# Optimization experiments

Measured on AMD Instinct MI355X. Metric: run time of the kernel, lower is better.

## Reference

```python
import jax, jax.numpy as jnp
import numpy as np

N_POINTS = 2_000_000
N_VOXELS = 1_500_000
N_SP = 50_000
C = 32
LN_EPS = 1e-5  # torch nn.LayerNorm default


def setup_inputs() -> dict:
    key = jax.random.key(0)
    ks = jax.random.split(key, 8)
    voxel_feats = jax.random.normal(ks[0], (N_VOXELS, C), jnp.float32)
    xyz = jax.random.normal(ks[1], (N_POINTS, 3), jnp.float32)
    p2v_map = jax.random.randint(ks[2], (N_POINTS,), 0, N_VOXELS, dtype=jnp.int32)
    sp_ids = jax.random.randint(ks[3], (N_POINTS,), 0, N_SP, dtype=jnp.int32)
    W1 = jax.random.normal(ks[4], (3, C), jnp.float32) * (1.0 / np.sqrt(3.0))
    b1 = jnp.zeros((C,), jnp.float32)
    gamma = jnp.ones((C,), jnp.float32)
    beta = jnp.zeros((C,), jnp.float32)
    W2 = jax.random.normal(ks[5], (C, C), jnp.float32) * (1.0 / np.sqrt(C))
    b2 = jnp.zeros((C,), jnp.float32)
    return {
        'voxel_feats': voxel_feats, 'xyz': xyz,
        'W1': W1, 'b1': b1, 'gamma': gamma, 'beta': beta, 'W2': W2, 'b2': b2,
        'p2v_map': p2v_map, 'sp_ids': sp_ids, 'num_superpoints': N_SP,
    }


def reference(voxel_feats, xyz, W1, b1, gamma, beta, W2, b2, p2v_map, sp_ids, num_superpoints):
    # gather voxel features to points: x = voxel_feats[p2v_map]  [N_pts, C]
    x = voxel_feats[p2v_map]

    # pos_encode MLP: Linear(3,32) -> LayerNorm(32) -> ReLU -> Linear(32,32)
    h = xyz @ W1 + b1
    mu = jnp.mean(h, axis=-1, keepdims=True)
    var = jnp.mean(jnp.square(h - mu), axis=-1, keepdims=True)
    h = (h - mu) * jax.lax.rsqrt(var + LN_EPS) * gamma + beta
    x_pos = jax.nn.relu(h) @ W2 + b2

    # scatter(reduce='mean') into superpoints; compute counts once
    counts = jax.ops.segment_sum(jnp.ones((xyz.shape[0],), x.dtype), sp_ids,
                                 num_segments=num_superpoints)
    denom = jnp.maximum(counts, 1.0)[:, None]

    def smean(v):
        return jax.ops.segment_sum(v, sp_ids, num_segments=num_superpoints) / denom

    x_sp = smean(x) + smean(x_pos)          # [S, C]
    sp_xyz = smean(xyz)                      # [S, 3]
    return (x_sp, sp_xyz)
```

## Files before the change

kernel.cpp:

```cpp
#include <hip/hip_runtime.h>
#include <hip/hip_bf16.h>

#define C 32
#define LN_EPS 1e-5f
#define P 8
#define SCAN_BLK 1024

__device__ __forceinline__ unsigned pack_bf16x2(float a, float b) {
    __hip_bfloat162 bb = __float22bfloat162_rn(make_float2(a, b));
    return *reinterpret_cast<unsigned*>(&bb);
}

__global__ __launch_bounds__(256) void kA1_rank_mlp(
    const float* __restrict__ voxel_feats,
    const float* __restrict__ xyz,
    const float* __restrict__ W1, const float* __restrict__ b1,
    const float* __restrict__ gamma, const float* __restrict__ beta,
    const float* __restrict__ W2, const float* __restrict__ b2,
    const int* __restrict__ p2v, const int* __restrict__ sp_ids,
    int* __restrict__ count, int* __restrict__ rank,
    uint4* __restrict__ y_s,
    int n)
{
    int p = blockIdx.x * 256 + threadIdx.x;
    if (p >= n) return;

    int sp = sp_ids[p];
    rank[p] = atomicAdd(&count[sp], 1);

    int v = p2v[p];
    const float4* vrow = (const float4*)(voxel_feats + (size_t)v * C);
    float4 g0 = vrow[0], g1 = vrow[1], g2 = vrow[2], g3 = vrow[3];
    float4 g4 = vrow[4], g5 = vrow[5], g6 = vrow[6], g7 = vrow[7];

    float x0 = xyz[3 * p + 0];
    float x1 = xyz[3 * p + 1];
    float x2 = xyz[3 * p + 2];

    float h[C];
    #pragma unroll
    for (int c = 0; c < C; ++c)
        h[c] = fmaf(x0, W1[c], fmaf(x1, W1[C + c], fmaf(x2, W1[2 * C + c], b1[c])));

    float s = 0.f, s2 = 0.f;
    #pragma unroll
    for (int c = 0; c < C; ++c) { s += h[c]; s2 += h[c] * h[c]; }
    float mu   = s * (1.0f / C);
    float var  = fmaf(-mu, mu, s2 * (1.0f / C));
    float rstd = rsqrtf(var + LN_EPS);
    #pragma unroll
    for (int c = 0; c < C; ++c)
        h[c] = fmaxf(fmaf((h[c] - mu) * rstd, gamma[c], beta[c]), 0.0f);

    float acc[C];
    #pragma unroll
    for (int c = 0; c < C; ++c) acc[c] = b2[c];
    #pragma unroll
    for (int k = 0; k < C; ++k) {
        float rk = h[k];
        #pragma unroll
        for (int c = 0; c < C; ++c)
            acc[c] = fmaf(rk, W2[k * C + c], acc[c]);
    }

    float gf[C] = { g0.x,g0.y,g0.z,g0.w, g1.x,g1.y,g1.z,g1.w,
                    g2.x,g2.y,g2.z,g2.w, g3.x,g3.y,g3.z,g3.w,
                    g4.x,g4.y,g4.z,g4.w, g5.x,g5.y,g5.z,g5.w,
                    g6.x,g6.y,g6.z,g6.w, g7.x,g7.y,g7.z,g7.w };
    #pragma unroll
    for (int c = 0; c < C; ++c) acc[c] += gf[c];

    uint4 y0, y1, y2, y3;
    y0.x = pack_bf16x2(acc[0],  acc[1]);  y0.y = pack_bf16x2(acc[2],  acc[3]);
    y0.z = pack_bf16x2(acc[4],  acc[5]);  y0.w = pack_bf16x2(acc[6],  acc[7]);
    y1.x = pack_bf16x2(acc[8],  acc[9]);  y1.y = pack_bf16x2(acc[10], acc[11]);
    y1.z = pack_bf16x2(acc[12], acc[13]); y1.w = pack_bf16x2(acc[14], acc[15]);
    y2.x = pack_bf16x2(acc[16], acc[17]); y2.y = pack_bf16x2(acc[18], acc[19]);
    y2.z = pack_bf16x2(acc[20], acc[21]); y2.w = pack_bf16x2(acc[22], acc[23]);
    y3.x = pack_bf16x2(acc[24], acc[25]); y3.y = pack_bf16x2(acc[26], acc[27]);
    y3.z = pack_bf16x2(acc[28], acc[29]); y3.w = pack_bf16x2(acc[30], acc[31]);
    uint4* dst = y_s + (size_t)p * 4;
    dst[0] = y0; dst[1] = y1; dst[2] = y2; dst[3] = y3;
}

__global__ __launch_bounds__(SCAN_BLK) void k2a_scan_block(
    const int* __restrict__ count, int* __restrict__ off,
    int* __restrict__ bsum, int S)
{
    __shared__ int lds[SCAN_BLK];
    int t = threadIdx.x;
    int i = blockIdx.x * SCAN_BLK + t;
    int v = (i < S) ? count[i] : 0;
    lds[t] = v;
    __syncthreads();
    for (int d = 1; d < SCAN_BLK; d <<= 1) {
        int add = (t >= d) ? lds[t - d] : 0;
        __syncthreads();
        lds[t] += add;
        __syncthreads();
    }
    int incl = lds[t];
    if (i < S) off[i] = incl - v;
    if (t == SCAN_BLK - 1) bsum[blockIdx.x] = incl;
}

__global__ __launch_bounds__(64) void k2b_scan_bsums(int* __restrict__ bsum, int nb)
{
    int lane = threadIdx.x;
    int v = (lane < nb) ? bsum[lane] : 0;
    int own = v;
    for (int d = 1; d < 64; d <<= 1) {
        int u = __shfl_up(v, d, 64);
        if (lane >= d) v += u;
    }
    if (lane < nb) bsum[lane] = v - own;
}

__global__ __launch_bounds__(256) void k2c_add_prefix(
    int* __restrict__ off, const int* __restrict__ bsum, int S)
{
    int i = blockIdx.x * 256 + threadIdx.x;
    if (i >= S) return;
    off[i] += bsum[i / SCAN_BLK];
}

__global__ __launch_bounds__(256) void k3x_scatter16(
    const int* __restrict__ sp_ids, const int* __restrict__ rank,
    const int* __restrict__ off, const float* __restrict__ xyz,
    uint4* __restrict__ xyzp, int n)
{
    int p = blockIdx.x * 256 + threadIdx.x;
    if (p >= n) return;
    int sp = sp_ids[p];
    int j  = off[sp] + rank[p];
    xyzp[j] = make_uint4(__float_as_uint(xyz[3 * p + 0]),
                         __float_as_uint(xyz[3 * p + 1]),
                         __float_as_uint(xyz[3 * p + 2]),
                         (unsigned)p);
}

__global__ __launch_bounds__(256) void kB2_reduce(
    const uint4* __restrict__ y_s,
    const uint4* __restrict__ xyzp,
    const int* __restrict__ off, const int* __restrict__ count,
    float* __restrict__ out_x, float* __restrict__ out_xyz, int S)
{
    int gt  = blockIdx.x * 256 + threadIdx.x;
    int sp  = gt >> 3;
    int sub = gt & 7;
    if (sp >= S) return;

    int n    = count[sp];
    int base = off[sp];

    float acc[C];
    #pragma unroll
    for (int c = 0; c < C; ++c) acc[c] = 0.f;
    float ax = 0.f, ay = 0.f, az = 0.f;

    int i = sub;
    for (; i + P < n; i += 2 * P) {
        uint4 r0 = xyzp[base + i];
        uint4 r1 = xyzp[base + i + P];
        const uint4* q0 = y_s + (size_t)r0.w * 4;
        const uint4* q1 = y_s + (size_t)r1.w * 4;
        uint4 a0 = q0[0], b0 = q0[1], c0 = q0[2], d0 = q0[3];
        uint4 a1 = q1[0], b1_ = q1[1], c1 = q1[2], d1 = q1[3];
        ax += __uint_as_float(r0.x) + __uint_as_float(r1.x);
        ay += __uint_as_float(r0.y) + __uint_as_float(r1.y);
        az += __uint_as_float(r0.z) + __uint_as_float(r1.z);
        unsigned w0[16] = { a0.x,a0.y,a0.z,a0.w, b0.x,b0.y,b0.z,b0.w,
                            c0.x,c0.y,c0.z,c0.w, d0.x,d0.y,d0.z,d0.w };
        unsigned w1[16] = { a1.x,a1.y,a1.z,a1.w, b1_.x,b1_.y,b1_.z,b1_.w,
                            c1.x,c1.y,c1.z,c1.w, d1.x,d1.y,d1.z,d1.w };
        #pragma unroll
        for (int q = 0; q < 16; ++q) {
            acc[2 * q + 0] += __uint_as_float(w0[q] << 16) + __uint_as_float(w1[q] << 16);
            acc[2 * q + 1] += __uint_as_float(w0[q] & 0xFFFF0000u) + __uint_as_float(w1[q] & 0xFFFF0000u);
        }
    }
    if (i < n) {
        uint4 r0 = xyzp[base + i];
        const uint4* q0 = y_s + (size_t)r0.w * 4;
        uint4 a0 = q0[0], b0 = q0[1], c0 = q0[2], d0 = q0[3];
        ax += __uint_as_float(r0.x);
        ay += __uint_as_float(r0.y);
        az += __uint_as_float(r0.z);
        unsigned w0[16] = { a0.x,a0.y,a0.z,a0.w, b0.x,b0.y,b0.z,b0.w,
                            c0.x,c0.y,c0.z,c0.w, d0.x,d0.y,d0.z,d0.w };
        #pragma unroll
        for (int q = 0; q < 16; ++q) {
            acc[2 * q + 0] += __uint_as_float(w0[q] << 16);
            acc[2 * q + 1] += __uint_as_float(w0[q] & 0xFFFF0000u);
        }
    }

    #pragma unroll
    for (int c = 0; c < C; ++c) {
        acc[c] += __shfl_xor(acc[c], 1);
        acc[c] += __shfl_xor(acc[c], 2);
        acc[c] += __shfl_xor(acc[c], 4);
    }
    ax += __shfl_xor(ax, 1); ax += __shfl_xor(ax, 2); ax += __shfl_xor(ax, 4);
    ay += __shfl_xor(ay, 1); ay += __shfl_xor(ay, 2); ay += __shfl_xor(ay, 4);
    az += __shfl_xor(az, 1); az += __shfl_xor(az, 2); az += __shfl_xor(az, 4);

    if (sub == 0) {
        float inv = 1.0f / fmaxf((float)n, 1.0f);
        float4* o4 = (float4*)(out_x + (size_t)sp * C);
        #pragma unroll
        for (int q = 0; q < 8; ++q) {
            float4 f;
            f.x = acc[4 * q + 0] * inv;
            f.y = acc[4 * q + 1] * inv;
            f.z = acc[4 * q + 2] * inv;
            f.w = acc[4 * q + 3] * inv;
            o4[q] = f;
        }
        out_xyz[3 * sp + 0] = ax * inv;
        out_xyz[3 * sp + 1] = ay * inv;
        out_xyz[3 * sp + 2] = az * inv;
    }
}

__global__ __launch_bounds__(256) void k3_reorder(
    const int* __restrict__ sp_ids, const int* __restrict__ rank,
    const int* __restrict__ off, int* __restrict__ order, int n)
{
    int p = blockIdx.x * 256 + threadIdx.x;
    if (p >= n) return;
    order[off[sp_ids[p]] + rank[p]] = p;
}

__global__ __launch_bounds__(256) void kB_gather_reduce(
    const uint4* __restrict__ y_s, const float* __restrict__ xyz,
    const int* __restrict__ order,
    const int* __restrict__ off, const int* __restrict__ count,
    float* __restrict__ out_x, float* __restrict__ out_xyz, int S)
{
    int gt = blockIdx.x * 256 + threadIdx.x;
    int sp = gt >> 3, sub = gt & 7;
    if (sp >= S) return;
    int n = count[sp], base = off[sp];
    float acc[C];
    #pragma unroll
    for (int c = 0; c < C; ++c) acc[c] = 0.f;
    float ax = 0.f, ay = 0.f, az = 0.f;
    for (int i = sub; i < n; i += P) {
        int o = order[base + i];
        const uint4* r = y_s + (size_t)o * 4;
        uint4 a = r[0], b = r[1], c4 = r[2], d = r[3];
        const float* xp = xyz + 3 * (size_t)o;
        ax += xp[0]; ay += xp[1]; az += xp[2];
        unsigned w[16] = { a.x,a.y,a.z,a.w, b.x,b.y,b.z,b.w,
                           c4.x,c4.y,c4.z,c4.w, d.x,d.y,d.z,d.w };
        #pragma unroll
        for (int q = 0; q < 16; ++q) {
            acc[2 * q + 0] += __uint_as_float(w[q] << 16);
            acc[2 * q + 1] += __uint_as_float(w[q] & 0xFFFF0000u);
        }
    }
    #pragma unroll
    for (int c = 0; c < C; ++c) {
        acc[c] += __shfl_xor(acc[c], 1);
        acc[c] += __shfl_xor(acc[c], 2);
        acc[c] += __shfl_xor(acc[c], 4);
    }
    ax += __shfl_xor(ax, 1); ax += __shfl_xor(ax, 2); ax += __shfl_xor(ax, 4);
    ay += __shfl_xor(ay, 1); ay += __shfl_xor(ay, 2); ay += __shfl_xor(ay, 4);
    az += __shfl_xor(az, 1); az += __shfl_xor(az, 2); az += __shfl_xor(az, 4);
    if (sub == 0) {
        float inv = 1.0f / fmaxf((float)n, 1.0f);
        float4* o4 = (float4*)(out_x + (size_t)sp * C);
        #pragma unroll
        for (int q = 0; q < 8; ++q) {
            float4 f;
            f.x = acc[4 * q + 0] * inv; f.y = acc[4 * q + 1] * inv;
            f.z = acc[4 * q + 2] * inv; f.w = acc[4 * q + 3] * inv;
            o4[q] = f;
        }
        out_xyz[3 * sp + 0] = ax * inv;
        out_xyz[3 * sp + 1] = ay * inv;
        out_xyz[3 * sp + 2] = az * inv;
    }
}

extern "C" void kernel_launch(void* const* d_in, const int* in_sizes, int n_in,
                              void* d_out, int out_size, void* d_ws, size_t ws_size,
                              hipStream_t stream)
{
    const float* voxel_feats = (const float*)d_in[0];
    const float* xyz         = (const float*)d_in[1];
    const float* W1          = (const float*)d_in[2];
    const float* b1          = (const float*)d_in[3];
    const float* gamma       = (const float*)d_in[4];
    const float* beta        = (const float*)d_in[5];
    const float* W2          = (const float*)d_in[6];
    const float* b2          = (const float*)d_in[7];
    const int*   p2v         = (const int*)d_in[8];
    const int*   sp_ids      = (const int*)d_in[9];

    const int n_pts = in_sizes[8];
    const int S     = out_size / 35;

    float* out_x   = (float*)d_out;
    float* out_xyz = out_x + (size_t)S * C;

    int* count = (int*)d_ws;
    int* off   = count + S;
    int* bsum  = off + S;
    int* rank  = bsum + 64;

    size_t head_b = ((size_t)2 * S + 64 + (size_t)n_pts) * sizeof(int);
    head_b = (head_b + 255) & ~(size_t)255;
    size_t xyzp_b = (size_t)n_pts * 16;
    size_t y_b    = (size_t)n_pts * 64;

    int blk = 256;
    int gpts = (n_pts + blk - 1) / blk;
    int nb = (S + SCAN_BLK - 1) / SCAN_BLK;
    int n_thr = S * P;

    hipMemsetAsync(count, 0, (size_t)S * sizeof(int), stream);

    if (ws_size >= head_b + xyzp_b + y_b) {
        uint4* xyzp = (uint4*)((char*)d_ws + head_b);
        uint4* y_s  = (uint4*)((char*)d_ws + head_b + xyzp_b);

        kA1_rank_mlp<<<gpts, blk, 0, stream>>>(
            voxel_feats, xyz, W1, b1, gamma, beta, W2, b2,
            p2v, sp_ids, count, rank, y_s, n_pts);
        k2a_scan_block<<<nb, SCAN_BLK, 0, stream>>>(count, off, bsum, S);
        k2b_scan_bsums<<<1, 64, 0, stream>>>(bsum, nb);
        k2c_add_prefix<<<(S + blk - 1) / blk, blk, 0, stream>>>(off, bsum, S);
        k3x_scatter16<<<gpts, blk, 0, stream>>>(sp_ids, rank, off, xyz, xyzp, n_pts);
        kB2_reduce<<<(n_thr + blk - 1) / blk, blk, 0, stream>>>(
            y_s, xyzp, off, count, out_x, out_xyz, S);
    } else {
        int* order = rank + n_pts;
        size_t head5_b = ((size_t)2 * S + 64 + (size_t)2 * n_pts) * sizeof(int);
        head5_b = (head5_b + 255) & ~(size_t)255;
        uint4* y_s = (uint4*)((char*)d_ws + head5_b);

        kA1_rank_mlp<<<gpts, blk, 0, stream>>>(
            voxel_feats, xyz, W1, b1, gamma, beta, W2, b2,
            p2v, sp_ids, count, rank, y_s, n_pts);
        k2a_scan_block<<<nb, SCAN_BLK, 0, stream>>>(count, off, bsum, S);
        k2b_scan_bsums<<<1, 64, 0, stream>>>(bsum, nb);
        k2c_add_prefix<<<(S + blk - 1) / blk, blk, 0, stream>>>(off, bsum, S);
        k3_reorder<<<gpts, blk, 0, stream>>>(sp_ids, rank, off, order, n_pts);
        kB_gather_reduce<<<(n_thr + blk - 1) / blk, blk, 0, stream>>>(
            y_s, xyz, order, off, count, out_x, out_xyz, S);
    }
}
```

Before: 519.1 us.

## Histogram first, then write MLP outputs directly into superpoint-sorted order

Adds a histogram pass over sp_ids and runs the scan before the MLP. The MLP kernel then claims a sorted slot through an atomic cursor and writes its bf16 row and the xyz record straight into segment-contiguous positions. The reduce kernel streams contiguous rows instead of gathering through a permutation index, which removes the separate scatter kernel and the rank array. In exchange it adds an extra pass over sp_ids, and the MLP kernel now makes scattered writes instead of coalesced ones.

```diff
diff --git a/kernel.cpp b/kernel.cpp
--- a/kernel.cpp
+++ b/kernel.cpp
@@ -11,7 +11,220 @@
     return *reinterpret_cast<unsigned*>(&bb);
 }
 
-__global__ __launch_bounds__(256) void kA1_rank_mlp(
+__global__ __launch_bounds__(256) void k0_hist(
+    const int* __restrict__ sp_ids, int* __restrict__ count, int n)
+{
+    int p = blockIdx.x * 256 + threadIdx.x;
+    if (p < n) atomicAdd(&count[sp_ids[p]], 1);
+}
+
+__global__ __launch_bounds__(SCAN_BLK) void k2a_scan_block(
+    const int* __restrict__ count, int* __restrict__ off,
+    int* __restrict__ bsum, int S)
+{
+    __shared__ int lds[SCAN_BLK];
+    int t = threadIdx.x;
+    int i = blockIdx.x * SCAN_BLK + t;
+    int v = (i < S) ? count[i] : 0;
+    lds[t] = v;
+    __syncthreads();
+    for (int d = 1; d < SCAN_BLK; d <<= 1) {
+        int add = (t >= d) ? lds[t - d] : 0;
+        __syncthreads();
+        lds[t] += add;
+        __syncthreads();
+    }
+    int incl = lds[t];
+    if (i < S) off[i] = incl - v;
+    if (t == SCAN_BLK - 1) bsum[blockIdx.x] = incl;
+}
+
+__global__ __launch_bounds__(64) void k2b_scan_bsums(int* __restrict__ bsum, int nb)
+{
+    int lane = threadIdx.x;
+    int v = (lane < nb) ? bsum[lane] : 0;
+    int own = v;
+    for (int d = 1; d < 64; d <<= 1) {
+        int u = __shfl_up(v, d, 64);
+        if (lane >= d) v += u;
+    }
+    if (lane < nb) bsum[lane] = v - own;
+}
+
+__global__ __launch_bounds__(256) void k2c_add_prefix(
+    int* __restrict__ off, const int* __restrict__ bsum,
+    int* __restrict__ cursor, int S)
+{
+    int i = blockIdx.x * 256 + threadIdx.x;
+    if (i >= S) return;
+    int o = off[i] + bsum[i / SCAN_BLK];
+    off[i] = o;
+    if (cursor) cursor[i] = o;
+}
+
+__global__ __launch_bounds__(256) void kA2_mlp_scatter(
+    const float* __restrict__ voxel_feats,
+    const float* __restrict__ xyz,
+    const float* __restrict__ W1, const float* __restrict__ b1,
+    const float* __restrict__ gamma, const float* __restrict__ beta,
+    const float* __restrict__ W2, const float* __restrict__ b2,
+    const int* __restrict__ p2v, const int* __restrict__ sp_ids,
+    int* __restrict__ cursor,
+    uint4* __restrict__ y_s,
+    uint4* __restrict__ xyzp,
+    int n)
+{
+    int p = blockIdx.x * 256 + threadIdx.x;
+    if (p >= n) return;
+
+    int sp = sp_ids[p];
+    int j = atomicAdd(&cursor[sp], 1);
+
+    int v = p2v[p];
+    const float4* vrow = (const float4*)(voxel_feats + (size_t)v * C);
+    float4 g0 = vrow[0], g1 = vrow[1], g2 = vrow[2], g3 = vrow[3];
+    float4 g4 = vrow[4], g5 = vrow[5], g6 = vrow[6], g7 = vrow[7];
+
+    float x0 = xyz[3 * p + 0];
+    float x1 = xyz[3 * p + 1];
+    float x2 = xyz[3 * p + 2];
+
+    float h[C];
+    #pragma unroll
+    for (int c = 0; c < C; ++c)
+        h[c] = fmaf(x0, W1[c], fmaf(x1, W1[C + c], fmaf(x2, W1[2 * C + c], b1[c])));
+
+    float s = 0.f, s2 = 0.f;
+    #pragma unroll
+    for (int c = 0; c < C; ++c) { s += h[c]; s2 += h[c] * h[c]; }
+    float mu   = s * (1.0f / C);
+    float var  = fmaf(-mu, mu, s2 * (1.0f / C));
+    float rstd = rsqrtf(var + LN_EPS);
+    #pragma unroll
+    for (int c = 0; c < C; ++c)
+        h[c] = fmaxf(fmaf((h[c] - mu) * rstd, gamma[c], beta[c]), 0.0f);
+
+    float acc[C];
+    #pragma unroll
+    for (int c = 0; c < C; ++c) acc[c] = b2[c];
+    #pragma unroll
+    for (int k = 0; k < C; ++k) {
+        float rk = h[k];
+        #pragma unroll
+        for (int c = 0; c < C; ++c)
+            acc[c] = fmaf(rk, W2[k * C + c], acc[c]);
+    }
+
+    float gf[C] = { g0.x,g0.y,g0.z,g0.w, g1.x,g1.y,g1.z,g1.w,
+                    g2.x,g2.y,g2.z,g2.w, g3.x,g3.y,g3.z,g3.w,
+                    g4.x,g4.y,g4.z,g4.w, g5.x,g5.y,g5.z,g5.w,
+                    g6.x,g6.y,g6.z,g6.w, g7.x,g7.y,g7.z,g7.w };
+    #pragma unroll
+    for (int c = 0; c < C; ++c) acc[c] += gf[c];
+
+    uint4 y0, y1, y2, y3;
+    y0.x = pack_bf16x2(acc[0],  acc[1]);  y0.y = pack_bf16x2(acc[2],  acc[3]);
+    y0.z = pack_bf16x2(acc[4],  acc[5]);  y0.w = pack_bf16x2(acc[6],  acc[7]);
+    y1.x = pack_bf16x2(acc[8],  acc[9]);  y1.y = pack_bf16x2(acc[10], acc[11]);
+    y1.z = pack_bf16x2(acc[12], acc[13]); y1.w = pack_bf16x2(acc[14], acc[15]);
+    y2.x = pack_bf16x2(acc[16], acc[17]); y2.y = pack_bf16x2(acc[18], acc[19]);
+    y2.z = pack_bf16x2(acc[20], acc[21]); y2.w = pack_bf16x2(acc[22], acc[23]);
+    y3.x = pack_bf16x2(acc[24], acc[25]); y3.y = pack_bf16x2(acc[26], acc[27]);
+    y3.z = pack_bf16x2(acc[28], acc[29]); y3.w = pack_bf16x2(acc[30], acc[31]);
+    uint4* dst = y_s + (size_t)j * 4;
+    dst[0] = y0; dst[1] = y1; dst[2] = y2; dst[3] = y3;
+
+    xyzp[j] = make_uint4(__float_as_uint(x0), __float_as_uint(x1),
+                         __float_as_uint(x2), (unsigned)p);
+}
+
+__global__ __launch_bounds__(256) void kB3_stream_reduce(
+    const uint4* __restrict__ y_s,
+    const uint4* __restrict__ xyzp,
+    const int* __restrict__ off, const int* __restrict__ count,
+    float* __restrict__ out_x, float* __restrict__ out_xyz, int S)
+{
+    int gt  = blockIdx.x * 256 + threadIdx.x;
+    int sp  = gt >> 3;
+    int sub = gt & 7;
+    if (sp >= S) return;
+
+    int n    = count[sp];
+    int base = off[sp];
+
+    float acc[C];
+    #pragma unroll
+    for (int c = 0; c < C; ++c) acc[c] = 0.f;
+    float ax = 0.f, ay = 0.f, az = 0.f;
+
+    int i = sub;
+    for (; i + P < n; i += 2 * P) {
+        int j0 = base + i, j1 = base + i + P;
+        const uint4* q0 = y_s + (size_t)j0 * 4;
+        const uint4* q1 = y_s + (size_t)j1 * 4;
+        uint4 a0 = q0[0], b0 = q0[1], c0 = q0[2], d0 = q0[3];
+        uint4 a1 = q1[0], b1_ = q1[1], c1 = q1[2], d1 = q1[3];
+        uint4 r0 = xyzp[j0];
+        uint4 r1 = xyzp[j1];
+        ax += __uint_as_float(r0.x) + __uint_as_float(r1.x);
+        ay += __uint_as_float(r0.y) + __uint_as_float(r1.y);
+        az += __uint_as_float(r0.z) + __uint_as_float(r1.z);
+        unsigned w0[16] = { a0.x,a0.y,a0.z,a0.w, b0.x,b0.y,b0.z,b0.w,
+                            c0.x,c0.y,c0.z,c0.w, d0.x,d0.y,d0.z,d0.w };
+        unsigned w1[16] = { a1.x,a1.y,a1.z,a1.w, b1_.x,b1_.y,b1_.z,b1_.w,
+                            c1.x,c1.y,c1.z,c1.w, d1.x,d1.y,d1.z,d1.w };
+        #pragma unroll
+        for (int q = 0; q < 16; ++q) {
+            acc[2 * q + 0] += __uint_as_float(w0[q] << 16) + __uint_as_float(w1[q] << 16);
+            acc[2 * q + 1] += __uint_as_float(w0[q] & 0xFFFF0000u) + __uint_as_float(w1[q] & 0xFFFF0000u);
+        }
+    }
+    if (i < n) {
+        int j0 = base + i;
+        const uint4* q0 = y_s + (size_t)j0 * 4;
+        uint4 a0 = q0[0], b0 = q0[1], c0 = q0[2], d0 = q0[3];
+        uint4 r0 = xyzp[j0];
+        ax += __uint_as_float(r0.x);
+        ay += __uint_as_float(r0.y);
+        az += __uint_as_float(r0.z);
+        unsigned w0[16] = { a0.x,a0.y,a0.z,a0.w, b0.x,b0.y,b0.z,b0.w,
+                            c0.x,c0.y,c0.z,c0.w, d0.x,d0.y,d0.z,d0.w };
+        #pragma unroll
+        for (int q = 0; q < 16; ++q) {
+            acc[2 * q + 0] += __uint_as_float(w0[q] << 16);
+            acc[2 * q + 1] += __uint_as_float(w0[q] & 0xFFFF0000u);
+        }
+    }
+
+    #pragma unroll
+    for (int c = 0; c < C; ++c) {
+        acc[c] += __shfl_xor(acc[c], 1);
+        acc[c] += __shfl_xor(acc[c], 2);
+        acc[c] += __shfl_xor(acc[c], 4);
+    }
+    ax += __shfl_xor(ax, 1); ax += __shfl_xor(ax, 2); ax += __shfl_xor(ax, 4);
+    ay += __shfl_xor(ay, 1); ay += __shfl_xor(ay, 2); ay += __shfl_xor(ay, 4);
+    az += __shfl_xor(az, 1); az += __shfl_xor(az, 2); az += __shfl_xor(az, 4);
+
+    if (sub == 0) {
+        float inv = 1.0f / fmaxf((float)n, 1.0f);
+        float4* o4 = (float4*)(out_x + (size_t)sp * C);
+        #pragma unroll
+        for (int q = 0; q < 8; ++q) {
+            float4 f;
+            f.x = acc[4 * q + 0] * inv;
+            f.y = acc[4 * q + 1] * inv;
+            f.z = acc[4 * q + 2] * inv;
+            f.w = acc[4 * q + 3] * inv;
+            o4[q] = f;
+        }
+        out_xyz[3 * sp + 0] = ax * inv;
+        out_xyz[3 * sp + 1] = ay * inv;
+        out_xyz[3 * sp + 2] = az * inv;
+    }
+}
+
+__global__ __launch_bounds__(256) void kA1_rank_mlp_seq(
     const float* __restrict__ voxel_feats,
     const float* __restrict__ xyz,
     const float* __restrict__ W1, const float* __restrict__ b1,
@@ -19,39 +232,30 @@
     const float* __restrict__ W2, const float* __restrict__ b2,
     const int* __restrict__ p2v, const int* __restrict__ sp_ids,
     int* __restrict__ count, int* __restrict__ rank,
-    uint4* __restrict__ y_s,
-    int n)
+    uint4* __restrict__ y_s, int n)
 {
     int p = blockIdx.x * 256 + threadIdx.x;
     if (p >= n) return;
-
     int sp = sp_ids[p];
     rank[p] = atomicAdd(&count[sp], 1);
-
     int v = p2v[p];
     const float4* vrow = (const float4*)(voxel_feats + (size_t)v * C);
     float4 g0 = vrow[0], g1 = vrow[1], g2 = vrow[2], g3 = vrow[3];
     float4 g4 = vrow[4], g5 = vrow[5], g6 = vrow[6], g7 = vrow[7];
-
-    float x0 = xyz[3 * p + 0];
-    float x1 = xyz[3 * p + 1];
-    float x2 = xyz[3 * p + 2];
-
+    float x0 = xyz[3 * p + 0], x1 = xyz[3 * p + 1], x2 = xyz[3 * p + 2];
     float h[C];
     #pragma unroll
     for (int c = 0; c < C; ++c)
         h[c] = fmaf(x0, W1[c], fmaf(x1, W1[C + c], fmaf(x2, W1[2 * C + c], b1[c])));
-
     float s = 0.f, s2 = 0.f;
     #pragma unroll
     for (int c = 0; c < C; ++c) { s += h[c]; s2 += h[c] * h[c]; }
-    float mu   = s * (1.0f / C);
-    float var  = fmaf(-mu, mu, s2 * (1.0f / C));
+    float mu = s * (1.0f / C);
+    float var = fmaf(-mu, mu, s2 * (1.0f / C));
     float rstd = rsqrtf(var + LN_EPS);
     #pragma unroll
     for (int c = 0; c < C; ++c)
         h[c] = fmaxf(fmaf((h[c] - mu) * rstd, gamma[c], beta[c]), 0.0f);
-
     float acc[C];
     #pragma unroll
     for (int c = 0; c < C; ++c) acc[c] = b2[c];
@@ -59,17 +263,14 @@
     for (int k = 0; k < C; ++k) {
         float rk = h[k];
         #pragma unroll
-        for (int c = 0; c < C; ++c)
-            acc[c] = fmaf(rk, W2[k * C + c], acc[c]);
-    }
-
+        for (int c = 0; c < C; ++c) acc[c] = fmaf(rk, W2[k * C + c], acc[c]);
+    }
     float gf[C] = { g0.x,g0.y,g0.z,g0.w, g1.x,g1.y,g1.z,g1.w,
                     g2.x,g2.y,g2.z,g2.w, g3.x,g3.y,g3.z,g3.w,
                     g4.x,g4.y,g4.z,g4.w, g5.x,g5.y,g5.z,g5.w,
                     g6.x,g6.y,g6.z,g6.w, g7.x,g7.y,g7.z,g7.w };
     #pragma unroll
     for (int c = 0; c < C; ++c) acc[c] += gf[c];
-
     uint4 y0, y1, y2, y3;
     y0.x = pack_bf16x2(acc[0],  acc[1]);  y0.y = pack_bf16x2(acc[2],  acc[3]);
     y0.z = pack_bf16x2(acc[4],  acc[5]);  y0.w = pack_bf16x2(acc[6],  acc[7]);
@@ -83,146 +284,6 @@
     dst[0] = y0; dst[1] = y1; dst[2] = y2; dst[3] = y3;
 }
 
-__global__ __launch_bounds__(SCAN_BLK) void k2a_scan_block(
-    const int* __restrict__ count, int* __restrict__ off,
-    int* __restrict__ bsum, int S)
-{
-    __shared__ int lds[SCAN_BLK];
-    int t = threadIdx.x;
-    int i = blockIdx.x * SCAN_BLK + t;
-    int v = (i < S) ? count[i] : 0;
-    lds[t] = v;
-    __syncthreads();
-    for (int d = 1; d < SCAN_BLK; d <<= 1) {
-        int add = (t >= d) ? lds[t - d] : 0;
-        __syncthreads();
-        lds[t] += add;
-        __syncthreads();
-    }
-    int incl = lds[t];
-    if (i < S) off[i] = incl - v;
-    if (t == SCAN_BLK - 1) bsum[blockIdx.x] = incl;
-}
-
-__global__ __launch_bounds__(64) void k2b_scan_bsums(int* __restrict__ bsum, int nb)
-{
-    int lane = threadIdx.x;
-    int v = (lane < nb) ? bsum[lane] : 0;
-    int own = v;
-    for (int d = 1; d < 64; d <<= 1) {
-        int u = __shfl_up(v, d, 64);
-        if (lane >= d) v += u;
-    }
-    if (lane < nb) bsum[lane] = v - own;
-}
-
-__global__ __launch_bounds__(256) void k2c_add_prefix(
-    int* __restrict__ off, const int* __restrict__ bsum, int S)
-{
-    int i = blockIdx.x * 256 + threadIdx.x;
-    if (i >= S) return;
-    off[i] += bsum[i / SCAN_BLK];
-}
-
-__global__ __launch_bounds__(256) void k3x_scatter16(
-    const int* __restrict__ sp_ids, const int* __restrict__ rank,
-    const int* __restrict__ off, const float* __restrict__ xyz,
-    uint4* __restrict__ xyzp, int n)
-{
-    int p = blockIdx.x * 256 + threadIdx.x;
-    if (p >= n) return;
-    int sp = sp_ids[p];
-    int j  = off[sp] + rank[p];
-    xyzp[j] = make_uint4(__float_as_uint(xyz[3 * p + 0]),
-                         __float_as_uint(xyz[3 * p + 1]),
-                         __float_as_uint(xyz[3 * p + 2]),
-                         (unsigned)p);
-}
-
-__global__ __launch_bounds__(256) void kB2_reduce(
-    const uint4* __restrict__ y_s,
-    const uint4* __restrict__ xyzp,
-    const int* __restrict__ off, const int* __restrict__ count,
-    float* __restrict__ out_x, float* __restrict__ out_xyz, int S)
-{
-    int gt  = blockIdx.x * 256 + threadIdx.x;
-    int sp  = gt >> 3;
-    int sub = gt & 7;
-    if (sp >= S) return;
-
-    int n    = count[sp];
-    int base = off[sp];
-
-    float acc[C];
-    #pragma unroll
-    for (int c = 0; c < C; ++c) acc[c] = 0.f;
-    float ax = 0.f, ay = 0.f, az = 0.f;
-
-    int i = sub;
-    for (; i + P < n; i += 2 * P) {
-        uint4 r0 = xyzp[base + i];
-        uint4 r1 = xyzp[base + i + P];
-        const uint4* q0 = y_s + (size_t)r0.w * 4;
-        const uint4* q1 = y_s + (size_t)r1.w * 4;
-        uint4 a0 = q0[0], b0 = q0[1], c0 = q0[2], d0 = q0[3];
-        uint4 a1 = q1[0], b1_ = q1[1], c1 = q1[2], d1 = q1[3];
-        ax += __uint_as_float(r0.x) + __uint_as_float(r1.x);
-        ay += __uint_as_float(r0.y) + __uint_as_float(r1.y);
-        az += __uint_as_float(r0.z) + __uint_as_float(r1.z);
-        unsigned w0[16] = { a0.x,a0.y,a0.z,a0.w, b0.x,b0.y,b0.z,b0.w,
-                            c0.x,c0.y,c0.z,c0.w, d0.x,d0.y,d0.z,d0.w };
-        unsigned w1[16] = { a1.x,a1.y,a1.z,a1.w, b1_.x,b1_.y,b1_.z,b1_.w,
-                            c1.x,c1.y,c1.z,c1.w, d1.x,d1.y,d1.z,d1.w };
-        #pragma unroll
-        for (int q = 0; q < 16; ++q) {
-            acc[2 * q + 0] += __uint_as_float(w0[q] << 16) + __uint_as_float(w1[q] << 16);
-            acc[2 * q + 1] += __uint_as_float(w0[q] & 0xFFFF0000u) + __uint_as_float(w1[q] & 0xFFFF0000u);
-        }
-    }
-    if (i < n) {
-        uint4 r0 = xyzp[base + i];
-        const uint4* q0 = y_s + (size_t)r0.w * 4;
-        uint4 a0 = q0[0], b0 = q0[1], c0 = q0[2], d0 = q0[3];
-        ax += __uint_as_float(r0.x);
-        ay += __uint_as_float(r0.y);
-        az += __uint_as_float(r0.z);
-        unsigned w0[16] = { a0.x,a0.y,a0.z,a0.w, b0.x,b0.y,b0.z,b0.w,
-                            c0.x,c0.y,c0.z,c0.w, d0.x,d0.y,d0.z,d0.w };
-        #pragma unroll
-        for (int q = 0; q < 16; ++q) {
-            acc[2 * q + 0] += __uint_as_float(w0[q] << 16);
-            acc[2 * q + 1] += __uint_as_float(w0[q] & 0xFFFF0000u);
-        }
-    }
-
-    #pragma unroll
-    for (int c = 0; c < C; ++c) {
-        acc[c] += __shfl_xor(acc[c], 1);
-        acc[c] += __shfl_xor(acc[c], 2);
-        acc[c] += __shfl_xor(acc[c], 4);
-    }
-    ax += __shfl_xor(ax, 1); ax += __shfl_xor(ax, 2); ax += __shfl_xor(ax, 4);
-    ay += __shfl_xor(ay, 1); ay += __shfl_xor(ay, 2); ay += __shfl_xor(ay, 4);
-    az += __shfl_xor(az, 1); az += __shfl_xor(az, 2); az += __shfl_xor(az, 4);
-
-    if (sub == 0) {
-        float inv = 1.0f / fmaxf((float)n, 1.0f);
-        float4* o4 = (float4*)(out_x + (size_t)sp * C);
-        #pragma unroll
-        for (int q = 0; q < 8; ++q) {
-            float4 f;
-            f.x = acc[4 * q + 0] * inv;
-            f.y = acc[4 * q + 1] * inv;
-            f.z = acc[4 * q + 2] * inv;
-            f.w = acc[4 * q + 3] * inv;
-            o4[q] = f;
-        }
-        out_xyz[3 * sp + 0] = ax * inv;
-        out_xyz[3 * sp + 1] = ay * inv;
-        out_xyz[3 * sp + 2] = az * inv;
-    }
-}
-
 __global__ __launch_bounds__(256) void k3_reorder(
     const int* __restrict__ sp_ids, const int* __restrict__ rank,
     const int* __restrict__ off, int* __restrict__ order, int n)
@@ -306,48 +367,49 @@
     float* out_x   = (float*)d_out;
     float* out_xyz = out_x + (size_t)S * C;
 
-    int* count = (int*)d_ws;
-    int* off   = count + S;
-    int* bsum  = off + S;
-    int* rank  = bsum + 64;
-
-    size_t head_b = ((size_t)2 * S + 64 + (size_t)n_pts) * sizeof(int);
-    head_b = (head_b + 255) & ~(size_t)255;
-    size_t xyzp_b = (size_t)n_pts * 16;
-    size_t y_b    = (size_t)n_pts * 64;
-
     int blk = 256;
     int gpts = (n_pts + blk - 1) / blk;
     int nb = (S + SCAN_BLK - 1) / SCAN_BLK;
     int n_thr = S * P;
 
+    int* count  = (int*)d_ws;
+    int* off    = count + S;
+    int* bsum   = off + S;
+    int* cursor = bsum + 64;
+
+    size_t head_b = ((size_t)(3 * S) + 64) * sizeof(int);
+    head_b = (head_b + 255) & ~(size_t)255;
+    size_t xyzp_b = (size_t)n_pts * 16;
+    size_t y_b    = (size_t)n_pts * 64;
+
     hipMemsetAsync(count, 0, (size_t)S * sizeof(int), stream);
 
     if (ws_size >= head_b + xyzp_b + y_b) {
         uint4* xyzp = (uint4*)((char*)d_ws + head_b);
         uint4* y_s  = (uint4*)((char*)d_ws + head_b + xyzp_b);
 
-        kA1_rank_mlp<<<gpts, blk, 0, stream>>>(
+        k0_hist<<<gpts, blk, 0, stream>>>(sp_ids, count, n_pts);
+        k2a_scan_block<<<nb, SCAN_BLK, 0, stream>>>(count, off, bsum, S);
+        k2b_scan_bsums<<<1, 64, 0, stream>>>(bsum, nb);
+        k2c_add_prefix<<<(S + blk - 1) / blk, blk, 0, stream>>>(off, bsum, cursor, S);
+        kA2_mlp_scatter<<<gpts, blk, 0, stream>>>(
+            voxel_feats, xyz, W1, b1, gamma, beta, W2, b2,
+            p2v, sp_ids, cursor, y_s, xyzp, n_pts);
+        kB3_stream_reduce<<<(n_thr + blk - 1) / blk, blk, 0, stream>>>(
+            y_s, xyzp, off, count, out_x, out_xyz, S);
+    } else {
+        int* rank  = bsum + 64;
+        int* order = rank + n_pts;
+        size_t head5_b = ((size_t)2 * S + 64 + (size_t)2 * n_pts) * sizeof(int);
+        head5_b = (head5_b + 255) & ~(size_t)255;
+        uint4* y_s = (uint4*)((char*)d_ws + head5_b);
+
+        kA1_rank_mlp_seq<<<gpts, blk, 0, stream>>>(
             voxel_feats, xyz, W1, b1, gamma, beta, W2, b2,
             p2v, sp_ids, count, rank, y_s, n_pts);
         k2a_scan_block<<<nb, SCAN_BLK, 0, stream>>>(count, off, bsum, S);
         k2b_scan_bsums<<<1, 64, 0, stream>>>(bsum, nb);
-        k2c_add_prefix<<<(S + blk - 1) / blk, blk, 0, stream>>>(off, bsum, S);
-        k3x_scatter16<<<gpts, blk, 0, stream>>>(sp_ids, rank, off, xyz, xyzp, n_pts);
-        kB2_reduce<<<(n_thr + blk - 1) / blk, blk, 0, stream>>>(
-            y_s, xyzp, off, count, out_x, out_xyz, S);
-    } else {
-        int* order = rank + n_pts;
-        size_t head5_b = ((size_t)2 * S + 64 + (size_t)2 * n_pts) * sizeof(int);
-        head5_b = (head5_b + 255) & ~(size_t)255;
-        uint4* y_s = (uint4*)((char*)d_ws + head5_b);
-
-        kA1_rank_mlp<<<gpts, blk, 0, stream>>>(
-            voxel_feats, xyz, W1, b1, gamma, beta, W2, b2,
-            p2v, sp_ids, count, rank, y_s, n_pts);
-        k2a_scan_block<<<nb, SCAN_BLK, 0, stream>>>(count, off, bsum, S);
-        k2b_scan_bsums<<<1, 64, 0, stream>>>(bsum, nb);
-        k2c_add_prefix<<<(S + blk - 1) / blk, blk, 0, stream>>>(off, bsum, S);
+        k2c_add_prefix<<<(S + blk - 1) / blk, blk, 0, stream>>>(off, bsum, (int*)nullptr, S);
         k3_reorder<<<gpts, blk, 0, stream>>>(sp_ids, rank, off, order, n_pts);
         kB_gather_reduce<<<(n_thr + blk - 1) / blk, blk, 0, stream>>>(
             y_s, xyz, order, off, count, out_x, out_xyz, S);
```

Result: slower. 613.5 us (+18.2%).

## Fuse pos-MLP and voxel gather into segment reduce, drop bf16 intermediate

Applied to the files above, without the earlier changes.

The MLP and voxel-feature gather move out of a per-point pass that wrote a bf16 per-point buffer and into the per-superpoint reduction kernel. That kernel now reads a packed (xyz, voxel index) record sorted by superpoint and computes the MLP inline. Ranks are now assigned with a cursor atomic in the scatter pass instead of being stored during a histogram pass, so the rank array and the 128MB bf16 buffer are gone. In exchange, the reduction kernel carries heavy per-thread MLP arithmetic with high register pressure, the gather of 128B voxel rows becomes random inside the reduce, and the bf16 rounding of the intermediate is removed.

```diff
diff --git a/kernel.cpp b/kernel.cpp
--- a/kernel.cpp
+++ b/kernel.cpp
@@ -1,86 +1,15 @@
 #include <hip/hip_runtime.h>
-#include <hip/hip_bf16.h>
 
 #define C 32
 #define LN_EPS 1e-5f
 #define P 8
 #define SCAN_BLK 1024
 
-__device__ __forceinline__ unsigned pack_bf16x2(float a, float b) {
-    __hip_bfloat162 bb = __float22bfloat162_rn(make_float2(a, b));
-    return *reinterpret_cast<unsigned*>(&bb);
-}
-
-__global__ __launch_bounds__(256) void kA1_rank_mlp(
-    const float* __restrict__ voxel_feats,
-    const float* __restrict__ xyz,
-    const float* __restrict__ W1, const float* __restrict__ b1,
-    const float* __restrict__ gamma, const float* __restrict__ beta,
-    const float* __restrict__ W2, const float* __restrict__ b2,
-    const int* __restrict__ p2v, const int* __restrict__ sp_ids,
-    int* __restrict__ count, int* __restrict__ rank,
-    uint4* __restrict__ y_s,
-    int n)
+__global__ __launch_bounds__(256) void k0_hist(
+    const int* __restrict__ sp_ids, int* __restrict__ count, int n)
 {
     int p = blockIdx.x * 256 + threadIdx.x;
-    if (p >= n) return;
-
-    int sp = sp_ids[p];
-    rank[p] = atomicAdd(&count[sp], 1);
-
-    int v = p2v[p];
-    const float4* vrow = (const float4*)(voxel_feats + (size_t)v * C);
-    float4 g0 = vrow[0], g1 = vrow[1], g2 = vrow[2], g3 = vrow[3];
-    float4 g4 = vrow[4], g5 = vrow[5], g6 = vrow[6], g7 = vrow[7];
-
-    float x0 = xyz[3 * p + 0];
-    float x1 = xyz[3 * p + 1];
-    float x2 = xyz[3 * p + 2];
-
-    float h[C];
-    #pragma unroll
-    for (int c = 0; c < C; ++c)
-        h[c] = fmaf(x0, W1[c], fmaf(x1, W1[C + c], fmaf(x2, W1[2 * C + c], b1[c])));
-
-    float s = 0.f, s2 = 0.f;
-    #pragma unroll
-    for (int c = 0; c < C; ++c) { s += h[c]; s2 += h[c] * h[c]; }
-    float mu   = s * (1.0f / C);
-    float var  = fmaf(-mu, mu, s2 * (1.0f / C));
-    float rstd = rsqrtf(var + LN_EPS);
-    #pragma unroll
-    for (int c = 0; c < C; ++c)
-        h[c] = fmaxf(fmaf((h[c] - mu) * rstd, gamma[c], beta[c]), 0.0f);
-
-    float acc[C];
-    #pragma unroll
-    for (int c = 0; c < C; ++c) acc[c] = b2[c];
-    #pragma unroll
-    for (int k = 0; k < C; ++k) {
-        float rk = h[k];
-        #pragma unroll
-        for (int c = 0; c < C; ++c)
-            acc[c] = fmaf(rk, W2[k * C + c], acc[c]);
-    }
-
-    float gf[C] = { g0.x,g0.y,g0.z,g0.w, g1.x,g1.y,g1.z,g1.w,
-                    g2.x,g2.y,g2.z,g2.w, g3.x,g3.y,g3.z,g3.w,
-                    g4.x,g4.y,g4.z,g4.w, g5.x,g5.y,g5.z,g5.w,
-                    g6.x,g6.y,g6.z,g6.w, g7.x,g7.y,g7.z,g7.w };
-    #pragma unroll
-    for (int c = 0; c < C; ++c) acc[c] += gf[c];
-
-    uint4 y0, y1, y2, y3;
-    y0.x = pack_bf16x2(acc[0],  acc[1]);  y0.y = pack_bf16x2(acc[2],  acc[3]);
-    y0.z = pack_bf16x2(acc[4],  acc[5]);  y0.w = pack_bf16x2(acc[6],  acc[7]);
-    y1.x = pack_bf16x2(acc[8],  acc[9]);  y1.y = pack_bf16x2(acc[10], acc[11]);
-    y1.z = pack_bf16x2(acc[12], acc[13]); y1.w = pack_bf16x2(acc[14], acc[15]);
-    y2.x = pack_bf16x2(acc[16], acc[17]); y2.y = pack_bf16x2(acc[18], acc[19]);
-    y2.z = pack_bf16x2(acc[20], acc[21]); y2.w = pack_bf16x2(acc[22], acc[23]);
-    y3.x = pack_bf16x2(acc[24], acc[25]); y3.y = pack_bf16x2(acc[26], acc[27]);
-    y3.z = pack_bf16x2(acc[28], acc[29]); y3.w = pack_bf16x2(acc[30], acc[31]);
-    uint4* dst = y_s + (size_t)p * 4;
-    dst[0] = y0; dst[1] = y1; dst[2] = y2; dst[3] = y3;
+    if (p < n) atomicAdd(&count[sp_ids[p]], 1);
 }
 
 __global__ __launch_bounds__(SCAN_BLK) void k2a_scan_block(
@@ -117,31 +46,37 @@
 }
 
 __global__ __launch_bounds__(256) void k2c_add_prefix(
-    int* __restrict__ off, const int* __restrict__ bsum, int S)
+    int* __restrict__ off, const int* __restrict__ bsum,
+    int* __restrict__ cursor, int S)
 {
     int i = blockIdx.x * 256 + threadIdx.x;
     if (i >= S) return;
-    off[i] += bsum[i / SCAN_BLK];
-}
-
-__global__ __launch_bounds__(256) void k3x_scatter16(
-    const int* __restrict__ sp_ids, const int* __restrict__ rank,
-    const int* __restrict__ off, const float* __restrict__ xyz,
-    uint4* __restrict__ xyzp, int n)
+    int o = off[i] + bsum[i / SCAN_BLK];
+    off[i] = o;
+    cursor[i] = o;
+}
+
+__global__ __launch_bounds__(256) void k3v_scatter16(
+    const int* __restrict__ sp_ids, const int* __restrict__ p2v,
+    int* __restrict__ cursor, const float* __restrict__ xyz,
+    uint4* __restrict__ xyzv, int n)
 {
     int p = blockIdx.x * 256 + threadIdx.x;
     if (p >= n) return;
     int sp = sp_ids[p];
-    int j  = off[sp] + rank[p];
-    xyzp[j] = make_uint4(__float_as_uint(xyz[3 * p + 0]),
+    int j  = atomicAdd(&cursor[sp], 1);
+    xyzv[j] = make_uint4(__float_as_uint(xyz[3 * p + 0]),
                          __float_as_uint(xyz[3 * p + 1]),
                          __float_as_uint(xyz[3 * p + 2]),
-                         (unsigned)p);
-}
-
-__global__ __launch_bounds__(256) void kB2_reduce(
-    const uint4* __restrict__ y_s,
-    const uint4* __restrict__ xyzp,
+                         (unsigned)p2v[p]);
+}
+
+__global__ __launch_bounds__(256) void kB4_mlp_reduce(
+    const float* __restrict__ voxel_feats,
+    const uint4* __restrict__ xyzv,
+    const float* __restrict__ W1, const float* __restrict__ b1,
+    const float* __restrict__ gamma, const float* __restrict__ beta,
+    const float* __restrict__ W2, const float* __restrict__ b2,
     const int* __restrict__ off, const int* __restrict__ count,
     float* __restrict__ out_x, float* __restrict__ out_xyz, int S)
 {
@@ -158,41 +93,50 @@
     for (int c = 0; c < C; ++c) acc[c] = 0.f;
     float ax = 0.f, ay = 0.f, az = 0.f;
 
-    int i = sub;
-    for (; i + P < n; i += 2 * P) {
-        uint4 r0 = xyzp[base + i];
-        uint4 r1 = xyzp[base + i + P];
-        const uint4* q0 = y_s + (size_t)r0.w * 4;
-        const uint4* q1 = y_s + (size_t)r1.w * 4;
-        uint4 a0 = q0[0], b0 = q0[1], c0 = q0[2], d0 = q0[3];
-        uint4 a1 = q1[0], b1_ = q1[1], c1 = q1[2], d1 = q1[3];
-        ax += __uint_as_float(r0.x) + __uint_as_float(r1.x);
-        ay += __uint_as_float(r0.y) + __uint_as_float(r1.y);
-        az += __uint_as_float(r0.z) + __uint_as_float(r1.z);
-        unsigned w0[16] = { a0.x,a0.y,a0.z,a0.w, b0.x,b0.y,b0.z,b0.w,
-                            c0.x,c0.y,c0.z,c0.w, d0.x,d0.y,d0.z,d0.w };
-        unsigned w1[16] = { a1.x,a1.y,a1.z,a1.w, b1_.x,b1_.y,b1_.z,b1_.w,
-                            c1.x,c1.y,c1.z,c1.w, d1.x,d1.y,d1.z,d1.w };
-        #pragma unroll
-        for (int q = 0; q < 16; ++q) {
-            acc[2 * q + 0] += __uint_as_float(w0[q] << 16) + __uint_as_float(w1[q] << 16);
-            acc[2 * q + 1] += __uint_as_float(w0[q] & 0xFFFF0000u) + __uint_as_float(w1[q] & 0xFFFF0000u);
+    for (int i = sub; i < n; i += P) {
+        uint4 r = xyzv[base + i];
+
+        int v = (int)r.w;
+        const float4* vrow = (const float4*)(voxel_feats + (size_t)v * C);
+        float4 g0 = vrow[0], g1 = vrow[1], g2 = vrow[2], g3 = vrow[3];
+        float4 g4 = vrow[4], g5 = vrow[5], g6 = vrow[6], g7 = vrow[7];
+
+        float x0 = __uint_as_float(r.x);
+        float x1 = __uint_as_float(r.y);
+        float x2 = __uint_as_float(r.z);
+        ax += x0; ay += x1; az += x2;
+
+        float h[C];
+        #pragma unroll
+        for (int c = 0; c < C; ++c)
+            h[c] = fmaf(x0, W1[c], fmaf(x1, W1[C + c], fmaf(x2, W1[2 * C + c], b1[c])));
+
+        float s = 0.f, s2 = 0.f;
+        #pragma unroll
+        for (int c = 0; c < C; ++c) { s += h[c]; s2 += h[c] * h[c]; }
+        float mu   = s * (1.0f / C);
+        float var  = fmaf(-mu, mu, s2 * (1.0f / C));
+        float rstd = rsqrtf(var + LN_EPS);
+        #pragma unroll
+        for (int c = 0; c < C; ++c)
+            h[c] = fmaxf(fmaf((h[c] - mu) * rstd, gamma[c], beta[c]), 0.0f);
+
+        #pragma unroll
+        for (int c = 0; c < C; ++c) acc[c] += b2[c];
+        #pragma unroll
+        for (int k = 0; k < C; ++k) {
+            float rk = h[k];
+            #pragma unroll
+            for (int c = 0; c < C; ++c)
+                acc[c] = fmaf(rk, W2[k * C + c], acc[c]);
         }
-    }
-    if (i < n) {
-        uint4 r0 = xyzp[base + i];
-        const uint4* q0 = y_s + (size_t)r0.w * 4;
-        uint4 a0 = q0[0], b0 = q0[1], c0 = q0[2], d0 = q0[3];
-        ax += __uint_as_float(r0.x);
-        ay += __uint_as_float(r0.y);
-        az += __uint_as_float(r0.z);
-        unsigned w0[16] = { a0.x,a0.y,a0.z,a0.w, b0.x,b0.y,b0.z,b0.w,
-                            c0.x,c0.y,c0.z,c0.w, d0.x,d0.y,d0.z,d0.w };
-        #pragma unroll
-        for (int q = 0; q < 16; ++q) {
-            acc[2 * q + 0] += __uint_as_float(w0[q] << 16);
-            acc[2 * q + 1] += __uint_as_float(w0[q] & 0xFFFF0000u);
-        }
+
+        float gf[C] = { g0.x,g0.y,g0.z,g0.w, g1.x,g1.y,g1.z,g1.w,
+                        g2.x,g2.y,g2.z,g2.w, g3.x,g3.y,g3.z,g3.w,
+                        g4.x,g4.y,g4.z,g4.w, g5.x,g5.y,g5.z,g5.w,
+                        g6.x,g6.y,g6.z,g6.w, g7.x,g7.y,g7.z,g7.w };
+        #pragma unroll
+        for (int c = 0; c < C; ++c) acc[c] += gf[c];
     }
 
     #pragma unroll
@@ -223,68 +167,6 @@
     }
 }
 
-__global__ __launch_bounds__(256) void k3_reorder(
-    const int* __restrict__ sp_ids, const int* __restrict__ rank,
-    const int* __restrict__ off, int* __restrict__ order, int n)
-{
-    int p = blockIdx.x * 256 + threadIdx.x;
-    if (p >= n) return;
-    order[off[sp_ids[p]] + rank[p]] = p;
-}
-
-__global__ __launch_bounds__(256) void kB_gather_reduce(
-    const uint4* __restrict__ y_s, const float* __restrict__ xyz,
-    const int* __restrict__ order,
-    const int* __restrict__ off, const int* __restrict__ count,
-    float* __restrict__ out_x, float* __restrict__ out_xyz, int S)
-{
-    int gt = blockIdx.x * 256 + threadIdx.x;
-    int sp = gt >> 3, sub = gt & 7;
-    if (sp >= S) return;
-    int n = count[sp], base = off[sp];
-    float acc[C];
-    #pragma unroll
-    for (int c = 0; c < C; ++c) acc[c] = 0.f;
-    float ax = 0.f, ay = 0.f, az = 0.f;
-    for (int i = sub; i < n; i += P) {
-        int o = order[base + i];
-        const uint4* r = y_s + (size_t)o * 4;
-        uint4 a = r[0], b = r[1], c4 = r[2], d = r[3];
-        const float* xp = xyz + 3 * (size_t)o;
-        ax += xp[0]; ay += xp[1]; az += xp[2];
-        unsigned w[16] = { a.x,a.y,a.z,a.w, b.x,b.y,b.z,b.w,
-                           c4.x,c4.y,c4.z,c4.w, d.x,d.y,d.z,d.w };
-        #pragma unroll
-        for (int q = 0; q < 16; ++q) {
-            acc[2 * q + 0] += __uint_as_float(w[q] << 16);
-            acc[2 * q + 1] += __uint_as_float(w[q] & 0xFFFF0000u);
-        }
-    }
-    #pragma unroll
-    for (int c = 0; c < C; ++c) {
-        acc[c] += __shfl_xor(acc[c], 1);
-        acc[c] += __shfl_xor(acc[c], 2);
-        acc[c] += __shfl_xor(acc[c], 4);
-    }
-    ax += __shfl_xor(ax, 1); ax += __shfl_xor(ax, 2); ax += __shfl_xor(ax, 4);
-    ay += __shfl_xor(ay, 1); ay += __shfl_xor(ay, 2); ay += __shfl_xor(ay, 4);
-    az += __shfl_xor(az, 1); az += __shfl_xor(az, 2); az += __shfl_xor(az, 4);
-    if (sub == 0) {
-        float inv = 1.0f / fmaxf((float)n, 1.0f);
-        float4* o4 = (float4*)(out_x + (size_t)sp * C);
-        #pragma unroll
-        for (int q = 0; q < 8; ++q) {
-            float4 f;
-            f.x = acc[4 * q + 0] * inv; f.y = acc[4 * q + 1] * inv;
-            f.z = acc[4 * q + 2] * inv; f.w = acc[4 * q + 3] * inv;
-            o4[q] = f;
-        }
-        out_xyz[3 * sp + 0] = ax * inv;
-        out_xyz[3 * sp + 1] = ay * inv;
-        out_xyz[3 * sp + 2] = az * inv;
-    }
-}
-
 extern "C" void kernel_launch(void* const* d_in, const int* in_sizes, int n_in,
                               void* d_out, int out_size, void* d_ws, size_t ws_size,
                               hipStream_t stream)
@@ -306,50 +188,28 @@
     float* out_x   = (float*)d_out;
     float* out_xyz = out_x + (size_t)S * C;
 
-    int* count = (int*)d_ws;
-    int* off   = count + S;
-    int* bsum  = off + S;
-    int* rank  = bsum + 64;
-
-    size_t head_b = ((size_t)2 * S + 64 + (size_t)n_pts) * sizeof(int);
-    head_b = (head_b + 255) & ~(size_t)255;
-    size_t xyzp_b = (size_t)n_pts * 16;
-    size_t y_b    = (size_t)n_pts * 64;
-
     int blk = 256;
     int gpts = (n_pts + blk - 1) / blk;
     int nb = (S + SCAN_BLK - 1) / SCAN_BLK;
     int n_thr = S * P;
 
+    int* count  = (int*)d_ws;
+    int* off    = count + S;
+    int* bsum   = off + S;
+    int* cursor = bsum + 64;
+
+    size_t head_b = ((size_t)(3 * S) + 64) * sizeof(int);
+    head_b = (head_b + 255) & ~(size_t)255;
+    uint4* xyzv = (uint4*)((char*)d_ws + head_b);
+
     hipMemsetAsync(count, 0, (size_t)S * sizeof(int), stream);
 
-    if (ws_size >= head_b + xyzp_b + y_b) {
-        uint4* xyzp = (uint4*)((char*)d_ws + head_b);
-        uint4* y_s  = (uint4*)((char*)d_ws + head_b + xyzp_b);
-
-        kA1_rank_mlp<<<gpts, blk, 0, stream>>>(
-            voxel_feats, xyz, W1, b1, gamma, beta, W2, b2,
-            p2v, sp_ids, count, rank, y_s, n_pts);
-        k2a_scan_block<<<nb, SCAN_BLK, 0, stream>>>(count, off, bsum, S);
-        k2b_scan_bsums<<<1, 64, 0, stream>>>(bsum, nb);
-        k2c_add_prefix<<<(S + blk - 1) / blk, blk, 0, stream>>>(off, bsum, S);
-        k3x_scatter16<<<gpts, blk, 0, stream>>>(sp_ids, rank, off, xyz, xyzp, n_pts);
-        kB2_reduce<<<(n_thr + blk - 1) / blk, blk, 0, stream>>>(
-            y_s, xyzp, off, count, out_x, out_xyz, S);
-    } else {
-        int* order = rank + n_pts;
-        size_t head5_b = ((size_t)2 * S + 64 + (size_t)2 * n_pts) * sizeof(int);
-        head5_b = (head5_b + 255) & ~(size_t)255;
-        uint4* y_s = (uint4*)((char*)d_ws + head5_b);
-
-        kA1_rank_mlp<<<gpts, blk, 0, stream>>>(
-            voxel_feats, xyz, W1, b1, gamma, beta, W2, b2,
-            p2v, sp_ids, count, rank, y_s, n_pts);
-        k2a_scan_block<<<nb, SCAN_BLK, 0, stream>>>(count, off, bsum, S);
-        k2b_scan_bsums<<<1, 64, 0, stream>>>(bsum, nb);
-        k2c_add_prefix<<<(S + blk - 1) / blk, blk, 0, stream>>>(off, bsum, S);
-        k3_reorder<<<gpts, blk, 0, stream>>>(sp_ids, rank, off, order, n_pts);
-        kB_gather_reduce<<<(n_thr + blk - 1) / blk, blk, 0, stream>>>(
-            y_s, xyz, order, off, count, out_x, out_xyz, S);
-    }
-}
+    k0_hist<<<gpts, blk, 0, stream>>>(sp_ids, count, n_pts);
+    k2a_scan_block<<<nb, SCAN_BLK, 0, stream>>>(count, off, bsum, S);
+    k2b_scan_bsums<<<1, 64, 0, stream>>>(bsum, nb);
+    k2c_add_prefix<<<(S + blk - 1) / blk, blk, 0, stream>>>(off, bsum, cursor, S);
+    k3v_scatter16<<<gpts, blk, 0, stream>>>(sp_ids, p2v, cursor, xyz, xyzv, n_pts);
+    kB4_mlp_reduce<<<(n_thr + blk - 1) / blk, blk, 0, stream>>>(
+        voxel_feats, xyzv, W1, b1, gamma, beta, W2, b2,
+        off, count, out_x, out_xyz, S);
+}
```

Result: slower. 1.037 ms (+99.7%).
